# Performance work log

Measured on AMD Instinct MI355X. Metric: run time of the kernel, lower is better.

Reference implementation:

```python
import jax, jax.numpy as jnp
import numpy as np

CLASS_NUM = 31
KERNEL_MUL = 2.0
KERNEL_NUM = 5


def setup_inputs() -> dict:
    key = jax.random.key(0)
    k1, k2, k3, k4 = jax.random.split(key, 4)
    source = jax.random.normal(k1, (2048, 2048), dtype=jnp.float32)
    target = jax.random.normal(k2, (2048, 2048), dtype=jnp.float32)
    s_label = jax.random.randint(k3, (2048,), 0, CLASS_NUM)
    t_label = jax.random.normal(k4, (2048, CLASS_NUM), dtype=jnp.float32)
    return {"source": source, "target": target, "s_label": s_label, "t_label": t_label}


def _mmd_loss(source, target, s_label, t_label):
    ns = source.shape[0]
    nt = target.shape[0]
    t_hard = jnp.argmax(t_label, axis=1)                       # hard target labels
    labels = jnp.concatenate([s_label, t_hard], axis=0)        # [N]
    total = jnp.concatenate([source, target], axis=0)          # [N, D]
    # pairwise squared euclidean distances via gram trick (same math as
    # ((x_i - x_j)**2).sum(-1), fused instead of the NxNxD expansion)
    sq = jnp.sum(total * total, axis=-1)                       # [N]
    D2 = sq[:, None] + sq[None, :] - 2.0 * (total @ total.T)   # [N, N]
    sign = jnp.concatenate([jnp.ones((ns,), D2.dtype), -jnp.ones((nt,), D2.dtype)])
    sign_pair = sign[:, None] * sign[None, :]                  # [N, N] (+SS,+TT,-ST,-TS)
    is_src = jnp.concatenate([jnp.ones((ns,), D2.dtype), jnp.zeros((nt,), D2.dtype)])
    bw_scale = KERNEL_MUL ** (KERNEL_NUM // 2)

    def per_class(carry, c):
        loss_acc, cnt = carry
        m = (labels == c).astype(D2.dtype)                     # [N]
        n_src = jnp.sum(m * is_src)
        n_tgt = jnp.sum(m * (1.0 - is_src))
        present = (n_src > 0) & (n_tgt > 0)                    # class in both domains
        n = n_src + n_tgt
        pair = m[:, None] * m[None, :]                         # [N, N] class mask
        # bandwidth from detached (.data) within-class distances
        l2sum = jax.lax.stop_gradient(jnp.sum(D2 * pair))
        denom = jnp.maximum(n * n - n, 1.0)
        bw = (l2sum / denom) / bw_scale
        bw = jnp.where(present, jnp.maximum(bw, 1e-20), 1.0)   # safe when absent
        K = jnp.zeros_like(D2)
        for i in range(KERNEL_NUM):
            K = K + jnp.exp(-D2 / (bw * (KERNEL_MUL ** i)))
        contrib = jnp.sum(pair * sign_pair * K) / jnp.maximum(n * n, 1.0)
        loss_acc = loss_acc + jnp.where(present, contrib, 0.0)
        cnt = cnt + jnp.where(present, 1.0, 0.0)
        return (loss_acc, cnt), None

    (loss, cnt), _ = jax.lax.scan(per_class, (jnp.float32(0.0), jnp.float32(0.0)),
                                  jnp.arange(CLASS_NUM))
    return loss / cnt


def reference(source, target, s_label, t_label):
    return _mmd_loss(source, target, s_label, t_label)
```

## Files before the change

kernel.cpp:

```cpp
#include <hip/hip_runtime.h>
#include <limits.h>

typedef __attribute__((ext_vector_type(8))) short bf16x8;
typedef __attribute__((ext_vector_type(4))) float f32x4;

#define TILE 32

__device__ __forceinline__ unsigned f2bf(float x) {
    unsigned u = __float_as_uint(x);
    return (u + 0x7fffu + ((u >> 16) & 1u)) >> 16;
}

__global__ void k_prep(const int* __restrict__ slab, const float* __restrict__ tlab,
                       int ns, int N, int C,
                       int* __restrict__ clsrows, int* __restrict__ cnt_src,
                       int* __restrict__ fill) {
    int i = blockIdx.x * 256 + threadIdx.x;
    if (i >= N) return;
    int lab;
    if (i < ns) {
        lab = slab[i];
    } else {
        const float* row = tlab + (size_t)(i - ns) * C;
        float best = row[0];
        lab = 0;
        for (int c = 1; c < C; c++) {
            float v = row[c];
            if (v > best) { best = v; lab = c; }
        }
    }
    if (i < ns) atomicAdd(&cnt_src[lab], 1);
    int pos = atomicAdd(&fill[lab], 1);
    clsrows[(size_t)lab * N + pos] = i;
}

__device__ __forceinline__ void scan_offsets2(const int* __restrict__ cnt_src,
                                              const int* __restrict__ fill, int C,
                                              int* proS, int* tpoS, int* tS, int* presS,
                                              int* padTotS, int* nTilesS) {
    if (threadIdx.x < 64) {
        int lane = threadIdx.x;
        int n = (lane < C) ? fill[lane] : 0;
        int nsrc = (lane < C) ? cnt_src[lane] : 0;
        int pres = (nsrc > 0 && (n - nsrc) > 0) ? 1 : 0;
        int T = pres ? (n + TILE - 1) / TILE : 0;
        int prw = T * 32;
        int t2 = T * (T + 1) / 2;
        int sp = prw, st = t2;
        for (int o = 1; o < 64; o <<= 1) {
            int a = __shfl_up(sp, o), b = __shfl_up(st, o);
            if (lane >= o) { sp += a; st += b; }
        }
        if (lane < C) {
            proS[lane] = sp - prw; tpoS[lane] = st - t2;
            tS[lane] = T; presS[lane] = pres;
        }
        if (lane == C - 1) { proS[C] = sp; tpoS[C] = st; *padTotS = sp; *nTilesS = st; }
    }
    __syncthreads();
}

__global__ __launch_bounds__(256) void k_gather(
        const float* __restrict__ src, const float* __restrict__ tgt,
        const int* __restrict__ clsrows,
        const int* __restrict__ cnt_src, const int* __restrict__ fill,
        int ns, int N, int D, int C,
        unsigned short* __restrict__ Xp, float* __restrict__ sqg, float* __restrict__ sgg,
        double* __restrict__ sqsum, float* __restrict__ classum) {
    __shared__ int proS[65], tpoS[65], tS[64], presS[64], padTotS, nTilesS;
    scan_offsets2(cnt_src, fill, C, proS, tpoS, tS, presS, &padTotS, &nTilesS);
    int p = blockIdx.x;
    int s0 = p * 16;
    if (s0 >= padTotS) return;
    int tid = threadIdx.x;
    int lane = tid & 63;
    int wv = tid >> 6;
    int c = __popcll(__ballot((lane < C) && (proS[lane] <= s0))) - 1;
    int n = fill[c];
    int idx0 = s0 - proS[c];

    __shared__ unsigned short Ls[16][2048 + 8];
    __shared__ float ls4[16][4];
    float cs[8];
    #pragma unroll
    for (int j = 0; j < 8; j++) cs[j] = 0.f;

    for (int r = 0; r < 16; r++) {
        int idx = idx0 + r;
        bool valid = idx < n;
        float4 v0 = {0.f, 0.f, 0.f, 0.f}, v1 = v0;
        if (valid) {
            int g = clsrows[(size_t)c * N + idx];
            const float* row = (g < ns) ? src + (size_t)g * D : tgt + (size_t)(g - ns) * D;
            v0 = *(const float4*)(row + tid * 8);
            v1 = *(const float4*)(row + tid * 8 + 4);
        }
        cs[0] += v0.x; cs[1] += v0.y; cs[2] += v0.z; cs[3] += v0.w;
        cs[4] += v1.x; cs[5] += v1.y; cs[6] += v1.z; cs[7] += v1.w;
        float a = v0.x*v0.x + v0.y*v0.y + v0.z*v0.z + v0.w*v0.w
                + v1.x*v1.x + v1.y*v1.y + v1.z*v1.z + v1.w*v1.w;
        for (int o = 32; o; o >>= 1) a += __shfl_down(a, o);
        if (lane == 0) ls4[r][wv] = a;
        uint4 pk;
        pk.x = f2bf(v0.x) | (f2bf(v0.y) << 16);
        pk.y = f2bf(v0.z) | (f2bf(v0.w) << 16);
        pk.z = f2bf(v1.x) | (f2bf(v1.y) << 16);
        pk.w = f2bf(v1.z) | (f2bf(v1.w) << 16);
        *(uint4*)&Ls[r][tid * 8] = pk;
    }
    #pragma unroll
    for (int j = 0; j < 8; j++)
        atomicAdd(&classum[(size_t)c * D + tid * 8 + j], cs[j]);
    __syncthreads();
    if (tid < 16) {
        int idx = idx0 + tid;
        bool valid = idx < n;
        float sq = ls4[tid][0] + ls4[tid][1] + ls4[tid][2] + ls4[tid][3];
        int g = valid ? clsrows[(size_t)c * N + idx] : 0;
        sqg[s0 + tid] = valid ? sq : 0.f;
        sgg[s0 + tid] = valid ? ((g < ns) ? 1.f : -1.f) : 0.f;
    }
    if (tid == 0) {
        double tot = 0.0;
        for (int r = 0; r < 16; r++)
            tot += (double)(ls4[r][0] + ls4[r][1] + ls4[r][2] + ls4[r][3]);
        atomicAdd(&sqsum[c], tot);
    }
    int pr = tid & 15, kq = tid >> 4;
    size_t pb = (size_t)p * 32768;
    for (int o = 0; o < 16; o++) {
        int k8 = kq * 16 + o;
        uint4 val = *(uint4*)&Ls[pr][k8 * 8];
        *(uint4*)(Xp + pb + (size_t)k8 * 128 + pr * 8) = val;
    }
}

__global__ void k_bw(const float* __restrict__ classum, const double* __restrict__ sqsum,
                     const int* __restrict__ cnt_src, const int* __restrict__ fill,
                     int D, int C, float* __restrict__ invbw) {
    int c = blockIdx.x;
    int tid = threadIdx.x;
    int n = fill[c], nsrc = cnt_src[c];
    int pres = (nsrc > 0 && (n - nsrc) > 0) ? 1 : 0;
    const float* cp = classum + (size_t)c * D;
    double sn = 0.0;
    for (int d = tid; d < D; d += 256) { double v = (double)cp[d]; sn += v * v; }
    for (int o = 32; o; o >>= 1) sn += __shfl_down(sn, o);
    __shared__ double ls[4];
    if ((tid & 63) == 0) ls[tid >> 6] = sn;
    __syncthreads();
    if (tid == 0) {
        double snorm = ls[0] + ls[1] + ls[2] + ls[3];
        double l2 = 2.0 * (double)n * sqsum[c] - 2.0 * snorm;
        double den = (double)n * (double)n - (double)n; if (den < 1.0) den = 1.0;
        double bw = l2 / den / 4.0;
        bw = pres ? fmax(bw, 1e-20) : 1.0;
        double m = 1.0;
        for (int k = 0; k < 5; k++) { invbw[c * 5 + k] = (float)(1.0 / (bw * m)); m *= 2.0; }
    }
}

__global__ __launch_bounds__(256) void k_pairs(
        const unsigned short* __restrict__ Xp, const float* __restrict__ sqg,
        const float* __restrict__ sgg, const float* __restrict__ invbw,
        const int* __restrict__ cnt_src, const int* __restrict__ fill,
        int N, int D, int C, double* __restrict__ contrib) {
    __shared__ int proS[65], tpoS[65], tS[64], presS[64], padTotS, nTilesS;
    scan_offsets2(cnt_src, fill, C, proS, tpoS, tS, presS, &padTotS, &nTilesS);
    __shared__ float Lp[4 * 16 * 64];
    __shared__ float sqA[32], sgA[32], sqB[32], sgB[32];

    int tid = threadIdx.x, lane = tid & 63, wv = tid >> 6;
    int kgrp = lane >> 4, lr = lane & 15;
    int nTiles = nTilesS;

    for (int job = blockIdx.x; job < nTiles; job += gridDim.x) {
        __syncthreads();
        int c = __popcll(__ballot((lane < C) && (tpoS[lane] <= job))) - 1;
        int t = job - tpoS[c];
        int T = tS[c];
        int ti = 0, rem = t;
        while (rem >= T - ti) { rem -= (T - ti); ti++; }
        int tj = ti + rem;
        int pbase = proS[c];
        int n = fill[c];
        float wgt = (ti == tj) ? 1.f : 2.f;

        if (tid < 32) {
            sqA[tid] = sqg[pbase + ti * 32 + tid];
            sgA[tid] = sgg[pbase + ti * 32 + tid];
        } else if (tid < 64) {
            int j = tid - 32;
            sqB[j] = sqg[pbase + tj * 32 + j];
            sgB[j] = sgg[pbase + tj * 32 + j];
        }

        size_t pA0 = ((size_t)(pbase >> 4) + ti * 2) * 32768;
        size_t pA1 = pA0 + 32768;
        size_t pB0 = ((size_t)(pbase >> 4) + tj * 2) * 32768;
        size_t pB1 = pB0 + 32768;
        int k8base = wv * 64;

        f32x4 a00 = (f32x4){0.f, 0.f, 0.f, 0.f}, a01 = a00, a10 = a00, a11 = a00;
        #pragma unroll 4
        for (int ks = 0; ks < 16; ks++) {
            size_t off = (size_t)(k8base + ks * 4 + kgrp) * 128 + lr * 8;
            bf16x8 va0 = *(const bf16x8*)(Xp + pA0 + off);
            bf16x8 va1 = *(const bf16x8*)(Xp + pA1 + off);
            bf16x8 vb0 = *(const bf16x8*)(Xp + pB0 + off);
            bf16x8 vb1 = *(const bf16x8*)(Xp + pB1 + off);
            a00 = __builtin_amdgcn_mfma_f32_16x16x32_bf16(va0, vb0, a00, 0, 0, 0);
            a01 = __builtin_amdgcn_mfma_f32_16x16x32_bf16(va0, vb1, a01, 0, 0, 0);
            a10 = __builtin_amdgcn_mfma_f32_16x16x32_bf16(va1, vb0, a10, 0, 0, 0);
            a11 = __builtin_amdgcn_mfma_f32_16x16x32_bf16(va1, vb1, a11, 0, 0, 0);
        }
        #pragma unroll
        for (int r = 0; r < 4; r++) {
            Lp[((wv * 4 + 0) * 4 + r) * 64 + lane] = a00[r];
            Lp[((wv * 4 + 1) * 4 + r) * 64 + lane] = a01[r];
            Lp[((wv * 4 + 2) * 4 + r) * 64 + lane] = a10[r];
            Lp[((wv * 4 + 3) * 4 + r) * 64 + lane] = a11[r];
        }
        __syncthreads();

        float ib0 = invbw[c * 5 + 0], ib1 = invbw[c * 5 + 1], ib2 = invbw[c * 5 + 2];
        float ib3 = invbw[c * 5 + 3], ib4 = invbw[c * 5 + 4];
        int i = tid >> 3;
        int j0 = (tid & 7) * 4;
        bool vi = (ti * 32 + i) < n;
        float sa = sqA[i], ga = sgA[i];
        float ts = 0.f;
        #pragma unroll
        for (int q = 0; q < 4; q++) {
            int j = j0 + q;
            bool vj = (tj * 32 + j) < n;
            int f = (i >> 4) * 2 + (j >> 4);
            int le = ((i & 15) >> 2) * 16 + (j & 15);
            int r = i & 3;
            float dot = Lp[((0 * 4 + f) * 4 + r) * 64 + le]
                      + Lp[((1 * 4 + f) * 4 + r) * 64 + le]
                      + Lp[((2 * 4 + f) * 4 + r) * 64 + le]
                      + Lp[((3 * 4 + f) * 4 + r) * 64 + le];
            if (vi && vj) {
                float D2 = sa + sqB[j] - 2.f * dot;
                float e = expf(-D2 * ib0) + expf(-D2 * ib1) + expf(-D2 * ib2)
                        + expf(-D2 * ib3) + expf(-D2 * ib4);
                ts += ga * sgB[j] * e;
            }
        }
        double ds = (double)(ts * wgt);
        for (int o = 32; o; o >>= 1) ds += __shfl_down(ds, o);
        if (lane == 0) atomicAdd(&contrib[c], ds);
    }
}

__global__ void k_final(const double* __restrict__ contrib,
                        const int* __restrict__ cnt_src, const int* __restrict__ fill,
                        int C, float* __restrict__ out) {
    int c = threadIdx.x;
    double l = 0.0, k = 0.0;
    if (c < C) {
        int n = fill[c], nsrc = cnt_src[c];
        if (nsrc > 0 && (n - nsrc) > 0) {
            double nn = (double)n * (double)n; if (nn < 1.0) nn = 1.0;
            l = contrib[c] / nn; k = 1.0;
        }
    }
    for (int o = 32; o; o >>= 1) { l += __shfl_down(l, o); k += __shfl_down(k, o); }
    if (c == 0) out[0] = (float)(l / k);
}

extern "C" void kernel_launch(void* const* d_in, const int* in_sizes, int n_in,
                              void* d_out, int out_size, void* d_ws, size_t ws_size,
                              hipStream_t stream) {
    const float* src  = (const float*)d_in[0];
    const float* tgt  = (const float*)d_in[1];
    const int*   slab = (const int*)d_in[2];
    const float* tlab = (const float*)d_in[3];
    const int ns = in_sizes[2];
    const int D  = in_sizes[0] / ns;
    const int nt = in_sizes[1] / D;
    const int C  = in_sizes[3] / nt;
    const int N  = ns + nt;
    const int padN = N + 32 * C;

    char* w = (char*)d_ws;
    size_t off = 0;
    auto take = [&](size_t bytes) -> char* {
        char* p = w + off;
        off = (off + bytes + 255) & ~(size_t)255;
        return p;
    };
    int*    cnt_src = (int*)take(64 * sizeof(int));
    int*    fill    = (int*)take(64 * sizeof(int));
    double* sqsum   = (double*)take(64 * sizeof(double));
    double* contrib = (double*)take(64 * sizeof(double));
    float*  classum = (float*)take((size_t)C * D * sizeof(float));
    size_t zbytes = off;
    int*            clsrows = (int*)take((size_t)C * N * sizeof(int));
    float*          sqg     = (float*)take((size_t)padN * sizeof(float));
    float*          sgg     = (float*)take((size_t)padN * sizeof(float));
    float*          invbw   = (float*)take((size_t)C * 5 * sizeof(float));
    unsigned short* Xp      = (unsigned short*)take((size_t)padN * D * sizeof(unsigned short));
    (void)n_in; (void)out_size; (void)ws_size;

    hipMemsetAsync(d_ws, 0, zbytes, stream);
    k_prep<<<(N + 255) / 256, 256, 0, stream>>>(slab, tlab, ns, N, C, clsrows, cnt_src, fill);
    k_gather<<<(padN + 15) / 16, 256, 0, stream>>>(src, tgt, clsrows, cnt_src, fill,
                                                   ns, N, D, C, Xp, sqg, sgg, sqsum, classum);
    k_bw<<<C, 256, 0, stream>>>(classum, sqsum, cnt_src, fill, D, C, invbw);
    k_pairs<<<1024, 256, 0, stream>>>(Xp, sqg, sgg, invbw, cnt_src, fill, N, D, C, contrib);
    k_final<<<1, 64, 0, stream>>>(contrib, cnt_src, fill, C, (float*)d_out);
}
```

Before: 142.0 us.

## Reduce class sums in shared memory and split pair-tile K across 8 waves

In the gather kernel, each wave now loads whole rows and accumulates per-class column sums into a shared-memory buffer. The buffer is then flushed to global memory with one atomic per column per block, instead of 8 global atomics per thread. The pair kernel moves to 512-thread blocks with 8 waves, each covering half the previous K range, and the grid is halved. This adds more partial-dot reductions through LDS and changes the occupancy and latency balance.

```diff
diff --git a/kernel.cpp b/kernel.cpp
--- a/kernel.cpp
+++ b/kernel.cpp
@@ -1,5 +1,4 @@
 #include <hip/hip_runtime.h>
-#include <limits.h>
 
 typedef __attribute__((ext_vector_type(8))) short bf16x8;
 typedef __attribute__((ext_vector_type(4))) float f32x4;
@@ -80,50 +79,64 @@
     int idx0 = s0 - proS[c];
 
     __shared__ unsigned short Ls[16][2048 + 8];
-    __shared__ float ls4[16][4];
-    float cs[8];
+    __shared__ float classumS[2048];
+    __shared__ float sqS[16];
+    for (int j = tid; j < 2048; j += 256) classumS[j] = 0.f;
+
+    float cs[4][8];
     #pragma unroll
-    for (int j = 0; j < 8; j++) cs[j] = 0.f;
-
-    for (int r = 0; r < 16; r++) {
+    for (int it = 0; it < 4; it++)
+        #pragma unroll
+        for (int j = 0; j < 8; j++) cs[it][j] = 0.f;
+
+    #pragma unroll
+    for (int rr = 0; rr < 4; rr++) {
+        int r = rr * 4 + wv;
         int idx = idx0 + r;
         bool valid = idx < n;
-        float4 v0 = {0.f, 0.f, 0.f, 0.f}, v1 = v0;
-        if (valid) {
-            int g = clsrows[(size_t)c * N + idx];
-            const float* row = (g < ns) ? src + (size_t)g * D : tgt + (size_t)(g - ns) * D;
-            v0 = *(const float4*)(row + tid * 8);
-            v1 = *(const float4*)(row + tid * 8 + 4);
-        }
-        cs[0] += v0.x; cs[1] += v0.y; cs[2] += v0.z; cs[3] += v0.w;
-        cs[4] += v1.x; cs[5] += v1.y; cs[6] += v1.z; cs[7] += v1.w;
-        float a = v0.x*v0.x + v0.y*v0.y + v0.z*v0.z + v0.w*v0.w
-                + v1.x*v1.x + v1.y*v1.y + v1.z*v1.z + v1.w*v1.w;
+        int g = valid ? clsrows[(size_t)c * N + idx] : 0;
+        const float* row = (g < ns) ? src + (size_t)g * D : tgt + (size_t)(g - ns) * D;
+        float a = 0.f;
+        #pragma unroll
+        for (int it = 0; it < 4; it++) {
+            float4 v0 = {0.f, 0.f, 0.f, 0.f}, v1 = v0;
+            if (valid) {
+                v0 = *(const float4*)(row + it * 512 + lane * 8);
+                v1 = *(const float4*)(row + it * 512 + lane * 8 + 4);
+            }
+            cs[it][0] += v0.x; cs[it][1] += v0.y; cs[it][2] += v0.z; cs[it][3] += v0.w;
+            cs[it][4] += v1.x; cs[it][5] += v1.y; cs[it][6] += v1.z; cs[it][7] += v1.w;
+            a += v0.x*v0.x + v0.y*v0.y + v0.z*v0.z + v0.w*v0.w
+               + v1.x*v1.x + v1.y*v1.y + v1.z*v1.z + v1.w*v1.w;
+            uint4 pk;
+            pk.x = f2bf(v0.x) | (f2bf(v0.y) << 16);
+            pk.y = f2bf(v0.z) | (f2bf(v0.w) << 16);
+            pk.z = f2bf(v1.x) | (f2bf(v1.y) << 16);
+            pk.w = f2bf(v1.z) | (f2bf(v1.w) << 16);
+            *(uint4*)&Ls[r][it * 512 + lane * 8] = pk;
+        }
         for (int o = 32; o; o >>= 1) a += __shfl_down(a, o);
-        if (lane == 0) ls4[r][wv] = a;
-        uint4 pk;
-        pk.x = f2bf(v0.x) | (f2bf(v0.y) << 16);
-        pk.y = f2bf(v0.z) | (f2bf(v0.w) << 16);
-        pk.z = f2bf(v1.x) | (f2bf(v1.y) << 16);
-        pk.w = f2bf(v1.z) | (f2bf(v1.w) << 16);
-        *(uint4*)&Ls[r][tid * 8] = pk;
-    }
+        if (lane == 0) sqS[r] = a;
+    }
+    __syncthreads();
     #pragma unroll
-    for (int j = 0; j < 8; j++)
-        atomicAdd(&classum[(size_t)c * D + tid * 8 + j], cs[j]);
+    for (int it = 0; it < 4; it++)
+        #pragma unroll
+        for (int j = 0; j < 8; j++)
+            atomicAdd(&classumS[it * 512 + lane * 8 + j], cs[it][j]);
     __syncthreads();
+    for (int j = tid; j < 2048; j += 256)
+        atomicAdd(&classum[(size_t)c * D + j], classumS[j]);
     if (tid < 16) {
         int idx = idx0 + tid;
         bool valid = idx < n;
-        float sq = ls4[tid][0] + ls4[tid][1] + ls4[tid][2] + ls4[tid][3];
         int g = valid ? clsrows[(size_t)c * N + idx] : 0;
-        sqg[s0 + tid] = valid ? sq : 0.f;
+        sqg[s0 + tid] = valid ? sqS[tid] : 0.f;
         sgg[s0 + tid] = valid ? ((g < ns) ? 1.f : -1.f) : 0.f;
     }
     if (tid == 0) {
         double tot = 0.0;
-        for (int r = 0; r < 16; r++)
-            tot += (double)(ls4[r][0] + ls4[r][1] + ls4[r][2] + ls4[r][3]);
+        for (int r = 0; r < 16; r++) tot += (double)sqS[r];
         atomicAdd(&sqsum[c], tot);
     }
     int pr = tid & 15, kq = tid >> 4;
@@ -160,14 +173,14 @@
     }
 }
 
-__global__ __launch_bounds__(256) void k_pairs(
+__global__ __launch_bounds__(512) void k_pairs(
         const unsigned short* __restrict__ Xp, const float* __restrict__ sqg,
         const float* __restrict__ sgg, const float* __restrict__ invbw,
         const int* __restrict__ cnt_src, const int* __restrict__ fill,
         int N, int D, int C, double* __restrict__ contrib) {
     __shared__ int proS[65], tpoS[65], tS[64], presS[64], padTotS, nTilesS;
     scan_offsets2(cnt_src, fill, C, proS, tpoS, tS, presS, &padTotS, &nTilesS);
-    __shared__ float Lp[4 * 16 * 64];
+    __shared__ float Lp[8 * 4 * 4 * 64];
     __shared__ float sqA[32], sgA[32], sqB[32], sgB[32];
 
     int tid = threadIdx.x, lane = tid & 63, wv = tid >> 6;
@@ -199,11 +212,11 @@
         size_t pA1 = pA0 + 32768;
         size_t pB0 = ((size_t)(pbase >> 4) + tj * 2) * 32768;
         size_t pB1 = pB0 + 32768;
-        int k8base = wv * 64;
+        int k8base = wv * 32;
 
         f32x4 a00 = (f32x4){0.f, 0.f, 0.f, 0.f}, a01 = a00, a10 = a00, a11 = a00;
-        #pragma unroll 4
-        for (int ks = 0; ks < 16; ks++) {
+        #pragma unroll
+        for (int ks = 0; ks < 8; ks++) {
             size_t off = (size_t)(k8base + ks * 4 + kgrp) * 128 + lr * 8;
             bf16x8 va0 = *(const bf16x8*)(Xp + pA0 + off);
             bf16x8 va1 = *(const bf16x8*)(Xp + pA1 + off);
@@ -225,22 +238,22 @@
 
         float ib0 = invbw[c * 5 + 0], ib1 = invbw[c * 5 + 1], ib2 = invbw[c * 5 + 2];
         float ib3 = invbw[c * 5 + 3], ib4 = invbw[c * 5 + 4];
-        int i = tid >> 3;
-        int j0 = (tid & 7) * 4;
+        int i = tid >> 4;
+        int j0 = (tid & 15) * 2;
         bool vi = (ti * 32 + i) < n;
         float sa = sqA[i], ga = sgA[i];
         float ts = 0.f;
         #pragma unroll
-        for (int q = 0; q < 4; q++) {
+        for (int q = 0; q < 2; q++) {
             int j = j0 + q;
             bool vj = (tj * 32 + j) < n;
             int f = (i >> 4) * 2 + (j >> 4);
             int le = ((i & 15) >> 2) * 16 + (j & 15);
             int r = i & 3;
-            float dot = Lp[((0 * 4 + f) * 4 + r) * 64 + le]
-                      + Lp[((1 * 4 + f) * 4 + r) * 64 + le]
-                      + Lp[((2 * 4 + f) * 4 + r) * 64 + le]
-                      + Lp[((3 * 4 + f) * 4 + r) * 64 + le];
+            float dot = 0.f;
+            #pragma unroll
+            for (int w8 = 0; w8 < 8; w8++)
+                dot += Lp[((w8 * 4 + f) * 4 + r) * 64 + le];
             if (vi && vj) {
                 float D2 = sa + sqB[j] - 2.f * dot;
                 float e = expf(-D2 * ib0) + expf(-D2 * ib1) + expf(-D2 * ib2)
@@ -309,6 +322,6 @@
     k_gather<<<(padN + 15) / 16, 256, 0, stream>>>(src, tgt, clsrows, cnt_src, fill,
                                                    ns, N, D, C, Xp, sqg, sgg, sqsum, classum);
     k_bw<<<C, 256, 0, stream>>>(classum, sqsum, cnt_src, fill, D, C, invbw);
-    k_pairs<<<1024, 256, 0, stream>>>(Xp, sqg, sgg, invbw, cnt_src, fill, N, D, C, contrib);
+    k_pairs<<<512, 512, 0, stream>>>(Xp, sqg, sgg, invbw, cnt_src, fill, N, D, C, contrib);
     k_final<<<1, 64, 0, stream>>>(contrib, cnt_src, fill, C, (float*)d_out);
 }
```

Result: slower. 156.4 us (+10.1%).

## Split gather kernel across feature chunks and move squared-norm sums to k_bw

Applied to the files above, without the earlier changes.

The gather kernel now runs on a 2D grid: each block handles 16 rows for one 512-wide feature chunk, so four times as many blocks each hold a much smaller LDS tile. Per-row squared norms are accumulated with atomics into a zeroed sqg buffer. Per-class column sums are now taken from the bf16-rounded values in LDS, with one atomic per column per block instead of eight per thread. The per-class sqsum double atomics are dropped; k_bw instead reduces sqg over each class's padded range. In exchange this adds more atomics, and the class sums lose precision from bf16 rounding, which can shift the bandwidth estimate.

```diff
diff --git a/kernel.cpp b/kernel.cpp
--- a/kernel.cpp
+++ b/kernel.cpp
@@ -1,5 +1,4 @@
 #include <hip/hip_runtime.h>
-#include <limits.h>
 
 typedef __attribute__((ext_vector_type(8))) short bf16x8;
 typedef __attribute__((ext_vector_type(4))) float f32x4;
@@ -66,92 +65,93 @@
         const int* __restrict__ cnt_src, const int* __restrict__ fill,
         int ns, int N, int D, int C,
         unsigned short* __restrict__ Xp, float* __restrict__ sqg, float* __restrict__ sgg,
-        double* __restrict__ sqsum, float* __restrict__ classum) {
+        float* __restrict__ classum) {
     __shared__ int proS[65], tpoS[65], tS[64], presS[64], padTotS, nTilesS;
     scan_offsets2(cnt_src, fill, C, proS, tpoS, tS, presS, &padTotS, &nTilesS);
     int p = blockIdx.x;
+    int chunk = blockIdx.y;
     int s0 = p * 16;
     if (s0 >= padTotS) return;
     int tid = threadIdx.x;
     int lane = tid & 63;
-    int wv = tid >> 6;
     int c = __popcll(__ballot((lane < C) && (proS[lane] <= s0))) - 1;
     int n = fill[c];
     int idx0 = s0 - proS[c];
-
-    __shared__ unsigned short Ls[16][2048 + 8];
-    __shared__ float ls4[16][4];
-    float cs[8];
+    int cbase = chunk * 512;
+
+    __shared__ unsigned short Ls[16][520];
+
+    int r = tid >> 4, q = tid & 15;
+    int idx = idx0 + r;
+    bool valid = idx < n;
+    int g = valid ? clsrows[(size_t)c * N + idx] : 0;
+    const float* row = (g < ns) ? src + (size_t)g * D : tgt + (size_t)(g - ns) * D;
+    float a = 0.f;
     #pragma unroll
-    for (int j = 0; j < 8; j++) cs[j] = 0.f;
-
-    for (int r = 0; r < 16; r++) {
-        int idx = idx0 + r;
-        bool valid = idx < n;
-        float4 v0 = {0.f, 0.f, 0.f, 0.f}, v1 = v0;
-        if (valid) {
-            int g = clsrows[(size_t)c * N + idx];
-            const float* row = (g < ns) ? src + (size_t)g * D : tgt + (size_t)(g - ns) * D;
-            v0 = *(const float4*)(row + tid * 8);
-            v1 = *(const float4*)(row + tid * 8 + 4);
-        }
-        cs[0] += v0.x; cs[1] += v0.y; cs[2] += v0.z; cs[3] += v0.w;
-        cs[4] += v1.x; cs[5] += v1.y; cs[6] += v1.z; cs[7] += v1.w;
-        float a = v0.x*v0.x + v0.y*v0.y + v0.z*v0.z + v0.w*v0.w
-                + v1.x*v1.x + v1.y*v1.y + v1.z*v1.z + v1.w*v1.w;
-        for (int o = 32; o; o >>= 1) a += __shfl_down(a, o);
-        if (lane == 0) ls4[r][wv] = a;
-        uint4 pk;
-        pk.x = f2bf(v0.x) | (f2bf(v0.y) << 16);
-        pk.y = f2bf(v0.z) | (f2bf(v0.w) << 16);
-        pk.z = f2bf(v1.x) | (f2bf(v1.y) << 16);
-        pk.w = f2bf(v1.z) | (f2bf(v1.w) << 16);
-        *(uint4*)&Ls[r][tid * 8] = pk;
-    }
+    for (int it = 0; it < 8; it++) {
+        int col = it * 64 + q * 4;
+        float4 v = {0.f, 0.f, 0.f, 0.f};
+        if (valid) v = *(const float4*)(row + cbase + col);
+        a += v.x * v.x + v.y * v.y + v.z * v.z + v.w * v.w;
+        uint2 pk;
+        pk.x = f2bf(v.x) | (f2bf(v.y) << 16);
+        pk.y = f2bf(v.z) | (f2bf(v.w) << 16);
+        *(uint2*)&Ls[r][col] = pk;
+    }
+    for (int o = 8; o; o >>= 1) a += __shfl_down(a, o, 16);
+    if (q == 0 && a != 0.f) atomicAdd(&sqg[s0 + r], a);
+    if (chunk == 0 && tid < 16) {
+        int idx2 = idx0 + tid;
+        bool v2 = idx2 < n;
+        int g2 = v2 ? clsrows[(size_t)c * N + idx2] : 0;
+        sgg[s0 + tid] = v2 ? ((g2 < ns) ? 1.f : -1.f) : 0.f;
+    }
+    __syncthreads();
+
     #pragma unroll
-    for (int j = 0; j < 8; j++)
-        atomicAdd(&classum[(size_t)c * D + tid * 8 + j], cs[j]);
-    __syncthreads();
-    if (tid < 16) {
-        int idx = idx0 + tid;
-        bool valid = idx < n;
-        float sq = ls4[tid][0] + ls4[tid][1] + ls4[tid][2] + ls4[tid][3];
-        int g = valid ? clsrows[(size_t)c * N + idx] : 0;
-        sqg[s0 + tid] = valid ? sq : 0.f;
-        sgg[s0 + tid] = valid ? ((g < ns) ? 1.f : -1.f) : 0.f;
-    }
-    if (tid == 0) {
-        double tot = 0.0;
-        for (int r = 0; r < 16; r++)
-            tot += (double)(ls4[r][0] + ls4[r][1] + ls4[r][2] + ls4[r][3]);
-        atomicAdd(&sqsum[c], tot);
-    }
-    int pr = tid & 15, kq = tid >> 4;
+    for (int h = 0; h < 2; h++) {
+        int d = h * 256 + tid;
+        float s = 0.f;
+        #pragma unroll
+        for (int rr = 0; rr < 16; rr++)
+            s += __uint_as_float((unsigned)Ls[rr][d] << 16);
+        if (s != 0.f) atomicAdd(&classum[(size_t)c * D + cbase + d], s);
+    }
+
+    int pr = tid & 15, k8g = tid >> 4;
     size_t pb = (size_t)p * 32768;
-    for (int o = 0; o < 16; o++) {
-        int k8 = kq * 16 + o;
-        uint4 val = *(uint4*)&Ls[pr][k8 * 8];
-        *(uint4*)(Xp + pb + (size_t)k8 * 128 + pr * 8) = val;
-    }
-}
-
-__global__ void k_bw(const float* __restrict__ classum, const double* __restrict__ sqsum,
+    #pragma unroll
+    for (int it = 0; it < 4; it++) {
+        int k8l = k8g * 4 + it;
+        uint4 val = *(uint4*)&Ls[pr][k8l * 8];
+        *(uint4*)(Xp + pb + (size_t)(chunk * 64 + k8l) * 128 + pr * 8) = val;
+    }
+}
+
+__global__ void k_bw(const float* __restrict__ classum, const float* __restrict__ sqg,
                      const int* __restrict__ cnt_src, const int* __restrict__ fill,
                      int D, int C, float* __restrict__ invbw) {
+    __shared__ int proS[65], tpoS[65], tS[64], presS[64], padTotS, nTilesS;
+    scan_offsets2(cnt_src, fill, C, proS, tpoS, tS, presS, &padTotS, &nTilesS);
     int c = blockIdx.x;
     int tid = threadIdx.x;
     int n = fill[c], nsrc = cnt_src[c];
     int pres = (nsrc > 0 && (n - nsrc) > 0) ? 1 : 0;
     const float* cp = classum + (size_t)c * D;
-    double sn = 0.0;
+    double sn = 0.0, sq = 0.0;
     for (int d = tid; d < D; d += 256) { double v = (double)cp[d]; sn += v * v; }
-    for (int o = 32; o; o >>= 1) sn += __shfl_down(sn, o);
-    __shared__ double ls[4];
-    if ((tid & 63) == 0) ls[tid >> 6] = sn;
+    for (int i = proS[c] + tid; i < proS[c + 1]; i += 256) sq += (double)sqg[i];
+    for (int o = 32; o; o >>= 1) {
+        sn += __shfl_down(sn, o);
+        sq += __shfl_down(sq, o);
+    }
+    __shared__ double ls[4], ls2[4];
+    if ((tid & 63) == 0) { ls[tid >> 6] = sn; ls2[tid >> 6] = sq; }
     __syncthreads();
     if (tid == 0) {
         double snorm = ls[0] + ls[1] + ls[2] + ls[3];
-        double l2 = 2.0 * (double)n * sqsum[c] - 2.0 * snorm;
+        double sqsum = ls2[0] + ls2[1] + ls2[2] + ls2[3];
+        double l2 = 2.0 * (double)n * sqsum - 2.0 * snorm;
         double den = (double)n * (double)n - (double)n; if (den < 1.0) den = 1.0;
         double bw = l2 / den / 4.0;
         bw = pres ? fmax(bw, 1e-20) : 1.0;
@@ -293,12 +293,11 @@
     };
     int*    cnt_src = (int*)take(64 * sizeof(int));
     int*    fill    = (int*)take(64 * sizeof(int));
-    double* sqsum   = (double*)take(64 * sizeof(double));
     double* contrib = (double*)take(64 * sizeof(double));
     float*  classum = (float*)take((size_t)C * D * sizeof(float));
+    float*  sqg     = (float*)take((size_t)padN * sizeof(float));
     size_t zbytes = off;
     int*            clsrows = (int*)take((size_t)C * N * sizeof(int));
-    float*          sqg     = (float*)take((size_t)padN * sizeof(float));
     float*          sgg     = (float*)take((size_t)padN * sizeof(float));
     float*          invbw   = (float*)take((size_t)C * 5 * sizeof(float));
     unsigned short* Xp      = (unsigned short*)take((size_t)padN * D * sizeof(unsigned short));
@@ -306,9 +305,10 @@
 
     hipMemsetAsync(d_ws, 0, zbytes, stream);
     k_prep<<<(N + 255) / 256, 256, 0, stream>>>(slab, tlab, ns, N, C, clsrows, cnt_src, fill);
-    k_gather<<<(padN + 15) / 16, 256, 0, stream>>>(src, tgt, clsrows, cnt_src, fill,
-                                                   ns, N, D, C, Xp, sqg, sgg, sqsum, classum);
-    k_bw<<<C, 256, 0, stream>>>(classum, sqsum, cnt_src, fill, D, C, invbw);
+    dim3 gg((padN + 15) / 16, 4);
+    k_gather<<<gg, 256, 0, stream>>>(src, tgt, clsrows, cnt_src, fill,
+                                     ns, N, D, C, Xp, sqg, sgg, classum);
+    k_bw<<<C, 256, 0, stream>>>(classum, sqg, cnt_src, fill, D, C, invbw);
     k_pairs<<<1024, 256, 0, stream>>>(Xp, sqg, sgg, invbw, cnt_src, fill, N, D, C, contrib);
     k_final<<<1, 64, 0, stream>>>(contrib, cnt_src, fill, C, (float*)d_out);
 }
```

Result: faster. 124.3 us (-12.5%).
